# Optimization experiments

Measured on AMD Instinct MI355X. Metric: run time of the kernel, lower is better.

## Reference

```python
import jax, jax.numpy as jnp
import numpy as np

N = 1024
X_DIM = 256
Y_DIM = 256
HIDDEN = 256


def setup_inputs() -> dict:
    key = jax.random.key(0)
    ks = jax.random.split(key, 6)
    lim1 = 1.0 / np.sqrt(X_DIM + Y_DIM)
    lim2 = 1.0 / np.sqrt(HIDDEN)
    return {
        "x_samples": jax.random.normal(ks[0], (N, X_DIM), jnp.float32),
        "y_samples": jax.random.normal(ks[1], (N, Y_DIM), jnp.float32),
        # F_func params: Linear(x_dim+y_dim, hidden) -> ReLU -> Linear(hidden, 1)
        "W1": jax.random.uniform(ks[2], (X_DIM + Y_DIM, HIDDEN), jnp.float32, -lim1, lim1),
        "b1": jax.random.uniform(ks[3], (HIDDEN,), jnp.float32, -lim1, lim1),
        "W2": jax.random.uniform(ks[4], (HIDDEN, 1), jnp.float32, -lim2, lim2),
        "b2": jax.random.uniform(ks[5], (1,), jnp.float32, -lim2, lim2),
    }


def reference(x_samples, y_samples, W1, b1, W2, b2):
    n = y_samples.shape[0]
    # Diagonal (joint) term: F([x_i, y_i])
    t0 = jnp.maximum(jnp.concatenate([x_samples, y_samples], axis=-1) @ W1 + b1, 0.0) @ W2 + b2  # [N,1]
    # Pairwise term: decompose first Linear into x- and y-projections, broadcast-sum.
    px = x_samples @ W1[:X_DIM]   # [N, H]
    py = y_samples @ W1[X_DIM:]   # [N, H]
    # torch layout: row axis = y tile, col axis = x tile -> h[i, j] = relu(py_i + px_j + b1)
    h = jnp.maximum(py[:, None, :] + px[None, :, :] + b1, 0.0)          # [N, N, H]
    t1 = jnp.einsum("yxh,ho->yx", h, W2) + b2[0] - 1.0                   # [N, N]
    # logsumexp over dim=1 (x axis), then exp-mean
    lse = jax.nn.logsumexp(t1, axis=1) - jnp.log(jnp.float32(n))         # [N]
    lower_bound = t0.mean() - jnp.exp(lse).mean()
    return lower_bound
```

## Files before the change

kernel.cpp:

```cpp
#include <hip/hip_runtime.h>

#define NS 1024
#define KD 256
#define H  256

__global__ __launch_bounds__(256) void proj_kernel(
    const float* __restrict__ X, const float* __restrict__ Y,
    const float* __restrict__ W1, const float* __restrict__ b1,
    float* __restrict__ PX, float* __restrict__ PYB)
{
    const int z = blockIdx.z;
    const float* __restrict__ A = z ? Y : X;
    const float* __restrict__ W = W1 + (z ? KD * H : 0);
    float* __restrict__ OUT = z ? PYB : PX;

    __shared__ float xs[32][36];
    __shared__ float ws[32][64];

    const int tid = threadIdx.x;
    const int tx = tid & 15;
    const int ty = tid >> 4;
    const int i0 = blockIdx.y * 32, h0 = blockIdx.x * 64;

    float acc[2][4] = {};

    for (int k0 = 0; k0 < KD; k0 += 32) {
        #pragma unroll
        for (int s = 0; s < 8; ++s) {
            int f = tid + 256 * s;
            int kk = f >> 6, hh = f & 63;
            ws[kk][hh] = W[(k0 + kk) * H + h0 + hh];
        }
        {
            int ii = tid & 31, q = tid >> 5;
            float4 v = *(const float4*)&A[(i0 + ii) * KD + k0 + q * 4];
            xs[q * 4 + 0][ii] = v.x;
            xs[q * 4 + 1][ii] = v.y;
            xs[q * 4 + 2][ii] = v.z;
            xs[q * 4 + 3][ii] = v.w;
        }
        __syncthreads();

        #pragma unroll
        for (int kk = 0; kk < 32; ++kk) {
            float xr[2];
            xr[0] = xs[kk][ty * 2 + 0];
            xr[1] = xs[kk][ty * 2 + 1];
            float wc[4];
            *(float4*)wc = *(const float4*)&ws[kk][tx * 4];
            #pragma unroll
            for (int r = 0; r < 2; ++r)
                #pragma unroll
                for (int c = 0; c < 4; ++c)
                    acc[r][c] = fmaf(xr[r], wc[c], acc[r][c]);
        }
        __syncthreads();
    }

    #pragma unroll
    for (int r = 0; r < 2; ++r) {
        const int row = i0 + ty * 2 + r;
        float o[4];
        #pragma unroll
        for (int c = 0; c < 4; ++c) o[c] = acc[r][c];
        if (z) {
            float bv[4];
            *(float4*)bv = *(const float4*)&b1[h0 + tx * 4];
            #pragma unroll
            for (int c = 0; c < 4; ++c) o[c] += bv[c];
        }
        *(float4*)&OUT[row * H + h0 + tx * 4] = *(float4*)o;
    }
}

__global__ __launch_bounds__(256) void pair_kernel(
    const float* __restrict__ PX, const float* __restrict__ PYB,
    const float* __restrict__ W2, const float* __restrict__ b2,
    float* __restrict__ eparts, float* __restrict__ dparts)
{
    __shared__ float pxt[64][68];
    __shared__ float pyt[64][36];
    __shared__ float w2s[H];
    __shared__ float red_e[256];
    __shared__ float red_d[256];

    const int tid = threadIdx.x;
    const int tx = tid & 15;
    const int ty = tid >> 4;
    const int j0 = blockIdx.x * 64, i0 = blockIdx.y * 32;

    w2s[tid] = W2[tid];

    const int jrow = tid & 63;
    const int jq   = tid >> 6;
    const int irow = tid & 31;
    const int iq   = tid >> 5;

    float acc[2][4] = {};

    for (int h0 = 0; h0 < H; h0 += 64) {
        __syncthreads();
        #pragma unroll
        for (int p = 0; p < 4; ++p) {
            const int hh = jq * 16 + p * 4;
            float4 vx = *(const float4*)&PX[(j0 + jrow) * H + h0 + hh];
            pxt[hh + 0][jrow] = vx.x; pxt[hh + 1][jrow] = vx.y;
            pxt[hh + 2][jrow] = vx.z; pxt[hh + 3][jrow] = vx.w;
        }
        #pragma unroll
        for (int p = 0; p < 2; ++p) {
            const int hh = iq * 8 + p * 4;
            float4 vy = *(const float4*)&PYB[(i0 + irow) * H + h0 + hh];
            pyt[hh + 0][irow] = vy.x; pyt[hh + 1][irow] = vy.y;
            pyt[hh + 2][irow] = vy.z; pyt[hh + 3][irow] = vy.w;
        }
        __syncthreads();

        #pragma unroll 4
        for (int hh4 = 0; hh4 < 64; hh4 += 4) {
            float w4[4];
            *(float4*)w4 = *(const float4*)&w2s[h0 + hh4];
            #pragma unroll
            for (int u = 0; u < 4; ++u) {
                const int hh = hh4 + u;
                float py2[2], px4[4];
                *(float2*)py2 = *(const float2*)&pyt[hh][ty * 2];
                *(float4*)px4 = *(const float4*)&pxt[hh][tx * 4];
                #pragma unroll
                for (int r = 0; r < 2; ++r)
                    #pragma unroll
                    for (int c = 0; c < 4; ++c) {
                        float s = py2[r] + px4[c];
                        acc[r][c] = fmaf(fmaxf(s, 0.f), w4[u], acc[r][c]);
                    }
            }
        }
    }

    const float c0 = b2[0] - 1.0f;
    float esum = 0.f, dsum = 0.f;
    #pragma unroll
    for (int r = 0; r < 2; ++r)
        #pragma unroll
        for (int c = 0; c < 4; ++c) {
            const float t1 = acc[r][c] + c0;
            esum += expf(t1);
            if (i0 + ty * 2 + r == j0 + tx * 4 + c) dsum += t1 + 1.0f;
        }

    __syncthreads();
    red_e[tid] = esum;
    red_d[tid] = dsum;
    __syncthreads();
    for (int s = 128; s > 0; s >>= 1) {
        if (tid < s) {
            red_e[tid] += red_e[tid + s];
            red_d[tid] += red_d[tid + s];
        }
        __syncthreads();
    }
    if (tid == 0) {
        const int bid = blockIdx.y * 16 + blockIdx.x;
        eparts[bid] = red_e[0];
        dparts[bid] = red_d[0];
    }
}

__global__ __launch_bounds__(256) void finalize_kernel(
    const float* __restrict__ eparts, const float* __restrict__ dparts,
    float* __restrict__ out)
{
    __shared__ double se[256];
    __shared__ double sd[256];
    const int t = threadIdx.x;
    se[t] = (double)eparts[t] + (double)eparts[t + 256];
    sd[t] = (double)dparts[t] + (double)dparts[t + 256];
    __syncthreads();
    for (int s = 128; s > 0; s >>= 1) {
        if (t < s) { se[t] += se[t + s]; sd[t] += sd[t + s]; }
        __syncthreads();
    }
    if (t == 0)
        out[0] = (float)(sd[0] / (double)NS - se[0] / ((double)NS * (double)NS));
}

extern "C" void kernel_launch(void* const* d_in, const int* in_sizes, int n_in,
                              void* d_out, int out_size, void* d_ws, size_t ws_size,
                              hipStream_t stream)
{
    const float* X  = (const float*)d_in[0];
    const float* Y  = (const float*)d_in[1];
    const float* W1 = (const float*)d_in[2];
    const float* b1 = (const float*)d_in[3];
    const float* W2 = (const float*)d_in[4];
    const float* b2 = (const float*)d_in[5];
    float* out = (float*)d_out;

    float* PX     = (float*)d_ws;
    float* PYB    = PX + NS * H;
    float* eparts = PYB + NS * H;
    float* dparts = eparts + 512;

    proj_kernel<<<dim3(H / 64, NS / 32, 2), 256, 0, stream>>>(X, Y, W1, b1, PX, PYB);
    pair_kernel<<<dim3(16, 32), 256, 0, stream>>>(PX, PYB, W2, b2, eparts, dparts);
    finalize_kernel<<<1, 256, 0, stream>>>(eparts, dparts, out);
}
```

Baseline: 106.0 us.

## Double-buffer pair tiles, widen j tile, fuse finalize via last-block reduction

The pair kernel now covers 128 columns per block, so each thread holds 16 accumulators, and it double-buffers the PX/PY shared tiles so the next h-chunk is staged while the current one is computed. The separate finalize kernel is removed: the last block, found through an atomic counter, does the final double-precision reduction. The projection kernel keeps the whole X row tile in shared memory and reads W1 straight from global memory, dropping the per-k-tile syncs. Risks are more registers and shared memory per block lowering occupancy, only 256 pair blocks for the GPU's compute units, and the counter reset relying on the ordering between kernels.

```diff
diff --git a/kernel.cpp b/kernel.cpp
--- a/kernel.cpp
+++ b/kernel.cpp
@@ -3,152 +3,163 @@
 #define NS 1024
 #define KD 256
 #define H  256
+#define NBLK 256
 
 __global__ __launch_bounds__(256) void proj_kernel(
     const float* __restrict__ X, const float* __restrict__ Y,
     const float* __restrict__ W1, const float* __restrict__ b1,
-    float* __restrict__ PX, float* __restrict__ PYB)
+    float* __restrict__ PX, float* __restrict__ PYB, int* __restrict__ counter)
 {
+    if (blockIdx.x == 0 && blockIdx.y == 0 && blockIdx.z == 0 && threadIdx.x == 0)
+        *counter = 0;
+
     const int z = blockIdx.z;
     const float* __restrict__ A = z ? Y : X;
     const float* __restrict__ W = W1 + (z ? KD * H : 0);
     float* __restrict__ OUT = z ? PYB : PX;
 
-    __shared__ float xs[32][36];
-    __shared__ float ws[32][64];
+    __shared__ float xs[KD][34];
 
     const int tid = threadIdx.x;
     const int tx = tid & 15;
     const int ty = tid >> 4;
     const int i0 = blockIdx.y * 32, h0 = blockIdx.x * 64;
 
+    {
+        const int ii = tid & 31, q = tid >> 5;
+        #pragma unroll
+        for (int u = 0; u < 8; ++u) {
+            const int k = u * 32 + q * 4;
+            float4 v = *(const float4*)&A[(i0 + ii) * KD + k];
+            xs[k + 0][ii] = v.x; xs[k + 1][ii] = v.y;
+            xs[k + 2][ii] = v.z; xs[k + 3][ii] = v.w;
+        }
+    }
+    __syncthreads();
+
     float acc[2][4] = {};
-
-    for (int k0 = 0; k0 < KD; k0 += 32) {
-        #pragma unroll
-        for (int s = 0; s < 8; ++s) {
-            int f = tid + 256 * s;
-            int kk = f >> 6, hh = f & 63;
-            ws[kk][hh] = W[(k0 + kk) * H + h0 + hh];
-        }
-        {
-            int ii = tid & 31, q = tid >> 5;
-            float4 v = *(const float4*)&A[(i0 + ii) * KD + k0 + q * 4];
-            xs[q * 4 + 0][ii] = v.x;
-            xs[q * 4 + 1][ii] = v.y;
-            xs[q * 4 + 2][ii] = v.z;
-            xs[q * 4 + 3][ii] = v.w;
-        }
-        __syncthreads();
-
-        #pragma unroll
-        for (int kk = 0; kk < 32; ++kk) {
-            float xr[2];
-            xr[0] = xs[kk][ty * 2 + 0];
-            xr[1] = xs[kk][ty * 2 + 1];
-            float wc[4];
-            *(float4*)wc = *(const float4*)&ws[kk][tx * 4];
-            #pragma unroll
-            for (int r = 0; r < 2; ++r)
-                #pragma unroll
-                for (int c = 0; c < 4; ++c)
-                    acc[r][c] = fmaf(xr[r], wc[c], acc[r][c]);
-        }
-        __syncthreads();
-    }
-
+    const float* __restrict__ wp = &W[h0 + tx * 4];
+
+    #pragma unroll 8
+    for (int k = 0; k < KD; ++k) {
+        float4 w4 = *(const float4*)&wp[k * H];
+        const float x0 = xs[k][ty * 2 + 0];
+        const float x1 = xs[k][ty * 2 + 1];
+        acc[0][0] = fmaf(x0, w4.x, acc[0][0]);
+        acc[0][1] = fmaf(x0, w4.y, acc[0][1]);
+        acc[0][2] = fmaf(x0, w4.z, acc[0][2]);
+        acc[0][3] = fmaf(x0, w4.w, acc[0][3]);
+        acc[1][0] = fmaf(x1, w4.x, acc[1][0]);
+        acc[1][1] = fmaf(x1, w4.y, acc[1][1]);
+        acc[1][2] = fmaf(x1, w4.z, acc[1][2]);
+        acc[1][3] = fmaf(x1, w4.w, acc[1][3]);
+    }
+
+    float bv[4] = {0.f, 0.f, 0.f, 0.f};
+    if (z) *(float4*)bv = *(const float4*)&b1[h0 + tx * 4];
     #pragma unroll
     for (int r = 0; r < 2; ++r) {
-        const int row = i0 + ty * 2 + r;
         float o[4];
         #pragma unroll
-        for (int c = 0; c < 4; ++c) o[c] = acc[r][c];
-        if (z) {
-            float bv[4];
-            *(float4*)bv = *(const float4*)&b1[h0 + tx * 4];
-            #pragma unroll
-            for (int c = 0; c < 4; ++c) o[c] += bv[c];
-        }
-        *(float4*)&OUT[row * H + h0 + tx * 4] = *(float4*)o;
+        for (int c = 0; c < 4; ++c) o[c] = acc[r][c] + bv[c];
+        *(float4*)&OUT[(i0 + ty * 2 + r) * H + h0 + tx * 4] = *(float4*)o;
     }
 }
+
+#define PXPAD 132
+#define PYPAD 34
 
 __global__ __launch_bounds__(256) void pair_kernel(
     const float* __restrict__ PX, const float* __restrict__ PYB,
     const float* __restrict__ W2, const float* __restrict__ b2,
-    float* __restrict__ eparts, float* __restrict__ dparts)
+    float* __restrict__ eparts, float* __restrict__ dparts,
+    int* __restrict__ counter, float* __restrict__ out)
 {
-    __shared__ float pxt[64][68];
-    __shared__ float pyt[64][36];
-    __shared__ float w2s[H];
-    __shared__ float red_e[256];
-    __shared__ float red_d[256];
+    __shared__ float pxt[2][64][PXPAD];
+    __shared__ float pyt[2][64][PYPAD];
+    __shared__ float red_e[256], red_d[256];
+    __shared__ double sde[256], sdd[256];
+    __shared__ int lastflag;
 
     const int tid = threadIdx.x;
     const int tx = tid & 15;
     const int ty = tid >> 4;
-    const int j0 = blockIdx.x * 64, i0 = blockIdx.y * 32;
-
-    w2s[tid] = W2[tid];
-
-    const int jrow = tid & 63;
-    const int jq   = tid >> 6;
-    const int irow = tid & 31;
-    const int iq   = tid >> 5;
-
-    float acc[2][4] = {};
-
-    for (int h0 = 0; h0 < H; h0 += 64) {
+    const int j0 = blockIdx.x * 128, i0 = blockIdx.y * 32;
+
+    const int su = tid & 7;
+    const int sjb = tid >> 3;
+    const int sii = tid & 31;
+    const int sq = tid >> 5;
+
+    float acc[2][8] = {};
+
+#define STAGE(T, B)                                                                  \
+    {                                                                                \
+        const int hb = (T) * 64;                                                     \
+        _Pragma("unroll")                                                            \
+        for (int t = 0; t < 4; ++t) {                                                \
+            _Pragma("unroll")                                                        \
+            for (int s = 0; s < 2; ++s) {                                            \
+                const int j = sjb + 32 * t;                                          \
+                const int hh = (su + 8 * s) * 4;                                     \
+                float4 v = *(const float4*)&PX[(j0 + j) * H + hb + hh];              \
+                pxt[B][hh + 0][j] = v.x; pxt[B][hh + 1][j] = v.y;                    \
+                pxt[B][hh + 2][j] = v.z; pxt[B][hh + 3][j] = v.w;                    \
+            }                                                                        \
+        }                                                                            \
+        _Pragma("unroll")                                                            \
+        for (int s = 0; s < 2; ++s) {                                                \
+            const int hh = sq * 8 + s * 4;                                           \
+            float4 v = *(const float4*)&PYB[(i0 + sii) * H + hb + hh];               \
+            pyt[B][hh + 0][sii] = v.x; pyt[B][hh + 1][sii] = v.y;                    \
+            pyt[B][hh + 2][sii] = v.z; pyt[B][hh + 3][sii] = v.w;                    \
+        }                                                                            \
+    }
+
+    STAGE(0, 0);
+    __syncthreads();
+
+    for (int t = 0; t < 4; ++t) {
+        const int cur = t & 1;
+        if (t < 3) {
+            if ((t & 1) == 0) STAGE(t + 1, 1)
+            else              STAGE(t + 1, 0)
+        }
+        const int hb = t * 64;
+        #pragma unroll 4
+        for (int hh = 0; hh < 64; ++hh) {
+            const float w = W2[hb + hh];
+            const float py0 = pyt[cur][hh][ty * 2 + 0];
+            const float py1 = pyt[cur][hh][ty * 2 + 1];
+            float a4[4], b4[4];
+            *(float4*)a4 = *(const float4*)&pxt[cur][hh][tx * 4];
+            *(float4*)b4 = *(const float4*)&pxt[cur][hh][64 + tx * 4];
+            #pragma unroll
+            for (int c = 0; c < 4; ++c) {
+                acc[0][c]     = fmaf(fmaxf(py0 + a4[c], 0.f), w, acc[0][c]);
+                acc[1][c]     = fmaf(fmaxf(py1 + a4[c], 0.f), w, acc[1][c]);
+                acc[0][4 + c] = fmaf(fmaxf(py0 + b4[c], 0.f), w, acc[0][4 + c]);
+                acc[1][4 + c] = fmaf(fmaxf(py1 + b4[c], 0.f), w, acc[1][4 + c]);
+            }
+        }
         __syncthreads();
-        #pragma unroll
-        for (int p = 0; p < 4; ++p) {
-            const int hh = jq * 16 + p * 4;
-            float4 vx = *(const float4*)&PX[(j0 + jrow) * H + h0 + hh];
-            pxt[hh + 0][jrow] = vx.x; pxt[hh + 1][jrow] = vx.y;
-            pxt[hh + 2][jrow] = vx.z; pxt[hh + 3][jrow] = vx.w;
-        }
-        #pragma unroll
-        for (int p = 0; p < 2; ++p) {
-            const int hh = iq * 8 + p * 4;
-            float4 vy = *(const float4*)&PYB[(i0 + irow) * H + h0 + hh];
-            pyt[hh + 0][irow] = vy.x; pyt[hh + 1][irow] = vy.y;
-            pyt[hh + 2][irow] = vy.z; pyt[hh + 3][irow] = vy.w;
-        }
-        __syncthreads();
-
-        #pragma unroll 4
-        for (int hh4 = 0; hh4 < 64; hh4 += 4) {
-            float w4[4];
-            *(float4*)w4 = *(const float4*)&w2s[h0 + hh4];
-            #pragma unroll
-            for (int u = 0; u < 4; ++u) {
-                const int hh = hh4 + u;
-                float py2[2], px4[4];
-                *(float2*)py2 = *(const float2*)&pyt[hh][ty * 2];
-                *(float4*)px4 = *(const float4*)&pxt[hh][tx * 4];
-                #pragma unroll
-                for (int r = 0; r < 2; ++r)
-                    #pragma unroll
-                    for (int c = 0; c < 4; ++c) {
-                        float s = py2[r] + px4[c];
-                        acc[r][c] = fmaf(fmaxf(s, 0.f), w4[u], acc[r][c]);
-                    }
-            }
-        }
     }
 
     const float c0 = b2[0] - 1.0f;
     float esum = 0.f, dsum = 0.f;
     #pragma unroll
-    for (int r = 0; r < 2; ++r)
+    for (int r = 0; r < 2; ++r) {
+        const int irow = i0 + ty * 2 + r;
         #pragma unroll
-        for (int c = 0; c < 4; ++c) {
-            const float t1 = acc[r][c] + c0;
-            esum += expf(t1);
-            if (i0 + ty * 2 + r == j0 + tx * 4 + c) dsum += t1 + 1.0f;
-        }
-
-    __syncthreads();
+        for (int g = 0; g < 2; ++g)
+            #pragma unroll
+            for (int c = 0; c < 4; ++c) {
+                const float t1 = acc[r][g * 4 + c] + c0;
+                esum += expf(t1);
+                if (irow == j0 + g * 64 + tx * 4 + c) dsum += t1 + 1.0f;
+            }
+    }
+
     red_e[tid] = esum;
     red_d[tid] = dsum;
     __syncthreads();
@@ -159,29 +170,29 @@
         }
         __syncthreads();
     }
+
+    const int bid = blockIdx.y * gridDim.x + blockIdx.x;
     if (tid == 0) {
-        const int bid = blockIdx.y * 16 + blockIdx.x;
-        eparts[bid] = red_e[0];
-        dparts[bid] = red_d[0];
-    }
-}
-
-__global__ __launch_bounds__(256) void finalize_kernel(
-    const float* __restrict__ eparts, const float* __restrict__ dparts,
-    float* __restrict__ out)
-{
-    __shared__ double se[256];
-    __shared__ double sd[256];
-    const int t = threadIdx.x;
-    se[t] = (double)eparts[t] + (double)eparts[t + 256];
-    sd[t] = (double)dparts[t] + (double)dparts[t + 256];
-    __syncthreads();
-    for (int s = 128; s > 0; s >>= 1) {
-        if (t < s) { se[t] += se[t + s]; sd[t] += sd[t + s]; }
+        __hip_atomic_store(&eparts[bid], red_e[0], __ATOMIC_RELAXED, __HIP_MEMORY_SCOPE_AGENT);
+        __hip_atomic_store(&dparts[bid], red_d[0], __ATOMIC_RELAXED, __HIP_MEMORY_SCOPE_AGENT);
+        __threadfence();
+        const int prev = __hip_atomic_fetch_add(counter, 1, __ATOMIC_ACQ_REL, __HIP_MEMORY_SCOPE_AGENT);
+        lastflag = (prev == NBLK - 1);
+    }
+    __syncthreads();
+
+    if (lastflag) {
+        __threadfence();
+        sde[tid] = (double)__hip_atomic_load(&eparts[tid], __ATOMIC_RELAXED, __HIP_MEMORY_SCOPE_AGENT);
+        sdd[tid] = (double)__hip_atomic_load(&dparts[tid], __ATOMIC_RELAXED, __HIP_MEMORY_SCOPE_AGENT);
         __syncthreads();
-    }
-    if (t == 0)
-        out[0] = (float)(sd[0] / (double)NS - se[0] / ((double)NS * (double)NS));
+        for (int s = 128; s > 0; s >>= 1) {
+            if (tid < s) { sde[tid] += sde[tid + s]; sdd[tid] += sdd[tid + s]; }
+            __syncthreads();
+        }
+        if (tid == 0)
+            out[0] = (float)(sdd[0] / (double)NS - sde[0] / ((double)NS * (double)NS));
+    }
 }
 
 extern "C" void kernel_launch(void* const* d_in, const int* in_sizes, int n_in,
@@ -199,9 +210,9 @@
     float* PX     = (float*)d_ws;
     float* PYB    = PX + NS * H;
     float* eparts = PYB + NS * H;
-    float* dparts = eparts + 512;
-
-    proj_kernel<<<dim3(H / 64, NS / 32, 2), 256, 0, stream>>>(X, Y, W1, b1, PX, PYB);
-    pair_kernel<<<dim3(16, 32), 256, 0, stream>>>(PX, PYB, W2, b2, eparts, dparts);
-    finalize_kernel<<<1, 256, 0, stream>>>(eparts, dparts, out);
+    float* dparts = eparts + 256;
+    int*   counter = (int*)(dparts + 256);
+
+    proj_kernel<<<dim3(H / 64, NS / 32, 2), 256, 0, stream>>>(X, Y, W1, b1, PX, PYB, counter);
+    pair_kernel<<<dim3(8, 32), 256, 0, stream>>>(PX, PYB, W2, b2, eparts, dparts, counter, out);
 }
```

Result: slower. 122.0 us (+15.1%).
